# Kernel tuning notes

Hardware: AMD Instinct MI355X
Metric: run time of the kernel (lower is better)

## Reference

```python
import jax, jax.numpy as jnp
import numpy as np

DIM = 4096
N_HEADS = 32
HEAD_DIM = 128
N_KV_HEADS = 8
KV_REPEATS = N_HEADS // N_KV_HEADS
SLIDING_WINDOW = 4096
SEQLEN = 2048
SCALE = HEAD_DIM ** -0.5
NEG = -1e9


def calculate_rope(x, cos, sin):
    # x: [S, H, D]; cos/sin: [S, D//2] applied to interleaved channel pairs
    x1, x2 = x[..., ::2], x[..., 1::2]
    c, s = cos[:, None, :], sin[:, None, :]
    r1 = x1 * c - x2 * s
    r2 = x1 * s + x2 * c
    return jnp.stack([r1, r2], axis=-1).reshape(x.shape)


def setup_inputs() -> dict:
    key = jax.random.key(0)
    ks = jax.random.split(key, 8)
    x = jax.random.normal(ks[0], (SEQLEN, DIM), dtype=jnp.float32)
    # rotary tables
    inv_freq = 1.0 / (10000.0 ** (np.arange(0, HEAD_DIM, 2, dtype=np.float32) / HEAD_DIM))
    t = np.arange(SEQLEN, dtype=np.float32)
    freqs = np.outer(t, inv_freq)  # [S, D/2]
    cos_freq = jnp.asarray(np.cos(freqs), dtype=jnp.float32)
    sin_freq = jnp.asarray(np.sin(freqs), dtype=jnp.float32)
    positions = jnp.arange(SEQLEN, dtype=jnp.int32)
    # causal sliding-window additive mask
    i = np.arange(SEQLEN)[:, None]
    j = np.arange(SEQLEN)[None, :]
    allow = (j <= i) & (j > i - SLIDING_WINDOW)
    mask = jnp.asarray(np.where(allow, 0.0, NEG), dtype=jnp.float32)
    cache_k = jnp.zeros((SLIDING_WINDOW, N_KV_HEADS, HEAD_DIM), dtype=jnp.float32)
    cache_v = jnp.zeros((SLIDING_WINDOW, N_KV_HEADS, HEAD_DIM), dtype=jnp.float32)
    # eqx.nn.Linear weights have shape (out_features, in_features)
    sd = DIM ** -0.5
    wq = jax.random.normal(ks[1], (N_HEADS * HEAD_DIM, DIM), dtype=jnp.float32) * sd
    wk = jax.random.normal(ks[2], (N_KV_HEADS * HEAD_DIM, DIM), dtype=jnp.float32) * sd
    wv = jax.random.normal(ks[3], (N_KV_HEADS * HEAD_DIM, DIM), dtype=jnp.float32) * sd
    wo = jax.random.normal(ks[4], (DIM, N_HEADS * HEAD_DIM), dtype=jnp.float32) * (N_HEADS * HEAD_DIM) ** -0.5
    return {"x": x, "cos_freq": cos_freq, "sin_freq": sin_freq, "positions": positions,
            "mask": mask, "cache_k": cache_k, "cache_v": cache_v,
            "wq": wq, "wk": wk, "wv": wv, "wo": wo}


def reference(x, cos_freq, sin_freq, positions, mask, cache_k, cache_v, wq, wk, wv, wo):
    seqlen = x.shape[0]
    xq = (x @ wq.T).reshape(seqlen, N_HEADS, HEAD_DIM)
    xk = (x @ wk.T).reshape(seqlen, N_KV_HEADS, HEAD_DIM)
    xv = (x @ wv.T).reshape(seqlen, N_KV_HEADS, HEAD_DIM)
    xq = calculate_rope(xq, cos_freq, sin_freq)
    xk = calculate_rope(xk, cos_freq, sin_freq)
    # prefill branch (positions.shape[0] > 1): scatter into sliding-window cache
    cache_k = cache_k.at[positions, :, :].set(xk[positions, :, :], mode='drop')
    cache_v = cache_v.at[positions, :, :].set(xv[positions, :, :], mode='drop')
    # GQA repeat kv heads
    k = jnp.repeat(xk, KV_REPEATS, axis=1)  # [S, H, D]
    v = jnp.repeat(xv, KV_REPEATS, axis=1)
    # scores: [H, Sq, Sk]
    scores = jnp.einsum('qhd,khd->hqk', xq, k) * SCALE
    scores = scores + mask[None, ...]
    probs = jax.nn.softmax(scores.astype(jnp.float32), axis=-1).astype(xq.dtype)
    out = jnp.einsum('hqk,khd->qhd', probs, v).reshape(seqlen, N_HEADS * HEAD_DIM)
    output = out @ wo.T
    return output, cache_k, cache_v
```

## Files before the change

kernel.cpp:

```cpp
#include <hip/hip_runtime.h>

typedef unsigned short ushort_t;
typedef unsigned int uint_t;
typedef __attribute__((ext_vector_type(8))) short bf16x8;
typedef __attribute__((ext_vector_type(4))) float floatx4;

#define SEQ 2048
#define DIM 4096
#define NH 32
#define NKV 8
#define HD 128
#define KVDIM 1024
#define QKVN 6144

__device__ __forceinline__ ushort_t f2b(float f) {
  union { float f; uint_t u; } x; x.f = f;
  uint_t u = x.u;
  u += 0x7fffu + ((u >> 16) & 1u);
  return (ushort_t)(u >> 16);
}

#define GLOAD_LDS(g, l) \
  __builtin_amdgcn_global_load_lds((const __attribute__((address_space(1))) void*)(g), \
                                   (__attribute__((address_space(3))) void*)(l), 16, 0, 0)

__global__ __launch_bounds__(256) void cvt_bf16(const float* __restrict__ src,
                                                ushort_t* __restrict__ dst, int n8) {
  int i = blockIdx.x * 256 + threadIdx.x;
  if (i >= n8) return;
  const float4* s = (const float4*)src;
  float4 a = s[2 * i], b = s[2 * i + 1];
  union { ushort_t u[8]; uint4 v; } o;
  o.u[0] = f2b(a.x); o.u[1] = f2b(a.y); o.u[2] = f2b(a.z); o.u[3] = f2b(a.w);
  o.u[4] = f2b(b.x); o.u[5] = f2b(b.y); o.u[6] = f2b(b.z); o.u[7] = f2b(b.w);
  ((uint4*)dst)[i] = o.v;
}

__global__ __launch_bounds__(256) void gemm128(const ushort_t* __restrict__ A,
                                               const ushort_t* __restrict__ B,
                                               float* __restrict__ C,
                                               int N, int K) {
  __shared__ __attribute__((aligned(16))) ushort_t lds_a[128 * 32];
  __shared__ __attribute__((aligned(16))) ushort_t lds_b[128 * 32];
  int tid = threadIdx.x;
  int lane = tid & 63;
  int w = tid >> 6;
  int m0 = blockIdx.y * 128, n0 = blockIdx.x * 128;
  int wm = (w >> 1) * 64, wn = (w & 1) * 64;
  int row = lane & 15, quad = lane >> 4;

  int sr = tid >> 2;
  int sc = (tid & 3) * 8;
  const ushort_t* Ag = A + (size_t)(m0 + sr) * K + sc;
  const ushort_t* Bg = B + (size_t)(n0 + sr) * K + sc;
  ushort_t* la0 = &lds_a[(tid & ~63) * 8];
  ushort_t* lb0 = &lds_b[(tid & ~63) * 8];

  floatx4 acc[4][4] = {};
  for (int k0 = 0; k0 < K; k0 += 32) {
    GLOAD_LDS(Ag + k0, la0);
    GLOAD_LDS(Ag + (size_t)64 * K + k0, la0 + 2048);
    GLOAD_LDS(Bg + k0, lb0);
    GLOAD_LDS(Bg + (size_t)64 * K + k0, lb0 + 2048);
    __syncthreads();
    bf16x8 af[4], bfr[4];
#pragma unroll
    for (int i = 0; i < 4; ++i) af[i] = *(const bf16x8*)&lds_a[(wm + i * 16 + row) * 32 + quad * 8];
#pragma unroll
    for (int j = 0; j < 4; ++j) bfr[j] = *(const bf16x8*)&lds_b[(wn + j * 16 + row) * 32 + quad * 8];
#pragma unroll
    for (int i = 0; i < 4; ++i)
#pragma unroll
      for (int j = 0; j < 4; ++j)
        acc[i][j] = __builtin_amdgcn_mfma_f32_16x16x32_bf16(af[i], bfr[j], acc[i][j], 0, 0, 0);
    __syncthreads();
  }
#pragma unroll
  for (int i = 0; i < 4; ++i)
#pragma unroll
    for (int j = 0; j < 4; ++j) {
      float* Cp = C + (size_t)(m0 + wm + i * 16 + quad * 4) * N + n0 + wn + j * 16 + row;
#pragma unroll
      for (int r = 0; r < 4; ++r) Cp[(size_t)r * N] = acc[i][j][r];
    }
}

__global__ __launch_bounds__(256) void rope_q(const float* __restrict__ qkv,
                                              const float* __restrict__ cosf,
                                              const float* __restrict__ sinf,
                                              ushort_t* __restrict__ qb) {
  int idx = blockIdx.x * 256 + threadIdx.x;
  int pos = idx >> 11;
  int p = idx & 2047;
  int h = p >> 6, i = p & 63;
  size_t sb = (size_t)pos * QKVN + h * HD + 2 * i;
  float x1 = qkv[sb], x2 = qkv[sb + 1];
  float c = cosf[pos * 64 + i], s = sinf[pos * 64 + i];
  float r1 = x1 * c - x2 * s;
  float r2 = x1 * s + x2 * c;
  size_t db = (size_t)pos * DIM + h * HD + 2 * i;
  ((uint_t*)qb)[db >> 1] = (uint_t)f2b(r1) | ((uint_t)f2b(r2) << 16);
}

__global__ __launch_bounds__(256) void rope_k(const float* __restrict__ qkv,
                                              const float* __restrict__ cosf,
                                              const float* __restrict__ sinf,
                                              ushort_t* __restrict__ kb,
                                              float* __restrict__ cache_k) {
  int idx = blockIdx.x * 256 + threadIdx.x;
  int pos = idx >> 9;
  int p = idx & 511;
  int kvh = p >> 6, i = p & 63;
  size_t sb = (size_t)pos * QKVN + DIM + kvh * HD + 2 * i;
  float x1 = qkv[sb], x2 = qkv[sb + 1];
  float c = cosf[pos * 64 + i], s = sinf[pos * 64 + i];
  float r1 = x1 * c - x2 * s;
  float r2 = x1 * s + x2 * c;
  size_t db = (size_t)pos * KVDIM + kvh * HD + 2 * i;
  ((uint_t*)kb)[db >> 1] = (uint_t)f2b(r1) | ((uint_t)f2b(r2) << 16);
  float2 cv; cv.x = r1; cv.y = r2;
  ((float2*)cache_k)[db >> 1] = cv;
}

__global__ __launch_bounds__(256) void vt_cache(const float* __restrict__ qkv,
                                                ushort_t* __restrict__ vtb,
                                                float* __restrict__ cache_v) {
  __shared__ float tile[64][65];
  int pos0 = blockIdx.x * 64, c0 = blockIdx.y * 64;
  int t = threadIdx.x;
  int pr = t >> 4, cq = (t & 15) * 4;
#pragma unroll
  for (int rr = 0; rr < 4; ++rr) {
    int prow = pr + rr * 16;
    float4 v = *(const float4*)(qkv + (size_t)(pos0 + prow) * QKVN + DIM + KVDIM + c0 + cq);
    *(float4*)(cache_v + (size_t)(pos0 + prow) * KVDIM + c0 + cq) = v;
    tile[prow][cq] = v.x; tile[prow][cq + 1] = v.y;
    tile[prow][cq + 2] = v.z; tile[prow][cq + 3] = v.w;
  }
  __syncthreads();
  int dc = t >> 2, pg = (t & 3) * 16;
  int kvh = c0 >> 7, dl = (c0 & 127) + dc;
  union { ushort_t u[16]; uint4 q[2]; } o;
#pragma unroll
  for (int e = 0; e < 16; ++e) o.u[e] = f2b(tile[pg + e][dc]);
  uint4* dst = (uint4*)(vtb + (size_t)kvh * (HD * SEQ) + (size_t)dl * SEQ + pos0 + pg);
  dst[0] = o.q[0]; dst[1] = o.q[1];
}

__global__ __launch_bounds__(256) void zero_tail(float* __restrict__ out) {
  int i = blockIdx.x * 256 + threadIdx.x;
  float4 z = {0.f, 0.f, 0.f, 0.f};
  ((float4*)(out + 10485760))[i] = z;
  ((float4*)(out + 14680064))[i] = z;
}

__global__ __launch_bounds__(256) void attn(const ushort_t* __restrict__ Q,
                                            const ushort_t* __restrict__ Kb,
                                            const ushort_t* __restrict__ Vt,
                                            ushort_t* __restrict__ O) {
  int qb = 31 - blockIdx.x;
  int h = blockIdx.y;
  int kvh = h >> 2;
  int tid = threadIdx.x;
  int w = tid >> 6, lane = tid & 63;
  int row = lane & 15, quad = lane >> 4;

  __shared__ __attribute__((aligned(16))) ushort_t lds_k[64][136];
  __shared__ __attribute__((aligned(16))) ushort_t lds_vt[128][72];
  __shared__ __attribute__((aligned(16))) float p_lds[4][16][68];

  int q0 = qb * 64 + w * 16;
  bf16x8 qf[4];
  const ushort_t* qp = Q + (size_t)(q0 + row) * DIM + h * HD + quad * 8;
#pragma unroll
  for (int ks = 0; ks < 4; ++ks) qf[ks] = *(const bf16x8*)(qp + ks * 32);

  floatx4 o_acc[8] = {};
  float l_r[4] = {0.f, 0.f, 0.f, 0.f};
  const float ssc = 0.08838834764831845f;

  int kr = tid >> 2, kc = (tid & 3) * 32;
  int vd = tid >> 1, vj = (tid & 1) * 32;
  const ushort_t* kg = Kb + (size_t)kr * KVDIM + kvh * HD + kc;
  const ushort_t* vg = Vt + (size_t)kvh * (HD * SEQ) + (size_t)vd * SEQ + vj;

  for (int kt = 0; kt <= qb; ++kt) {
    int kv0 = kt * 64;
#pragma unroll
    for (int e = 0; e < 4; ++e)
      *(bf16x8*)&lds_k[kr][kc + e * 8] = *(const bf16x8*)(kg + (size_t)kv0 * KVDIM + e * 8);
#pragma unroll
    for (int e = 0; e < 4; ++e)
      *(bf16x8*)&lds_vt[vd][vj + e * 8] = *(const bf16x8*)(vg + kv0 + e * 8);
    __syncthreads();

    floatx4 s[4] = {};
#pragma unroll
    for (int j2 = 0; j2 < 4; ++j2)
#pragma unroll
      for (int ks = 0; ks < 4; ++ks) {
        bf16x8 kfrag = *(const bf16x8*)&lds_k[j2 * 16 + row][ks * 32 + quad * 8];
        s[j2] = __builtin_amdgcn_mfma_f32_16x16x32_bf16(qf[ks], kfrag, s[j2], 0, 0, 0);
      }

    bool diag = (kt == qb);
    float pv[4][4];
#pragma unroll
    for (int j2 = 0; j2 < 4; ++j2)
#pragma unroll
      for (int r = 0; r < 4; ++r) {
        float v = s[j2][r] * ssc;
        if (diag) {
          int j_g = kv0 + j2 * 16 + row;
          int i_g = q0 + quad * 4 + r;
          v += (j_g <= i_g) ? 0.f : -1e9f;
        }
        float p = __expf(v);
        pv[j2][r] = p;
        l_r[r] += p;
      }
#pragma unroll
    for (int j2 = 0; j2 < 4; ++j2)
#pragma unroll
      for (int r = 0; r < 4; ++r) p_lds[w][quad * 4 + r][j2 * 16 + row] = pv[j2][r];
    bf16x8 pf[2];
#pragma unroll
    for (int kb = 0; kb < 2; ++kb) {
      union { bf16x8 v; ushort_t u[8]; } pu;
#pragma unroll
      for (int jj = 0; jj < 8; ++jj) pu.u[jj] = f2b(p_lds[w][row][kb * 32 + quad * 8 + jj]);
      pf[kb] = pu.v;
    }
#pragma unroll
    for (int db = 0; db < 8; ++db)
#pragma unroll
      for (int kb = 0; kb < 2; ++kb) {
        bf16x8 vfrag = *(const bf16x8*)&lds_vt[db * 16 + row][kb * 32 + quad * 8];
        o_acc[db] = __builtin_amdgcn_mfma_f32_16x16x32_bf16(pf[kb], vfrag, o_acc[db], 0, 0, 0);
      }
    __syncthreads();
  }

#pragma unroll
  for (int off = 1; off < 16; off <<= 1)
#pragma unroll
    for (int r = 0; r < 4; ++r) l_r[r] += __shfl_xor(l_r[r], off, 64);
  float inv[4];
#pragma unroll
  for (int r = 0; r < 4; ++r) inv[r] = 1.0f / l_r[r];
#pragma unroll
  for (int db = 0; db < 8; ++db)
#pragma unroll
    for (int r = 0; r < 4; ++r)
      O[(size_t)(q0 + quad * 4 + r) * DIM + h * HD + db * 16 + row] = f2b(o_acc[db][r] * inv[r]);
}

extern "C" void kernel_launch(void* const* d_in, const int* in_sizes, int n_in,
                              void* d_out, int out_size, void* d_ws, size_t ws_size,
                              hipStream_t stream) {
  const float* x    = (const float*)d_in[0];
  const float* cosf = (const float*)d_in[1];
  const float* sinf = (const float*)d_in[2];
  const float* wq = (const float*)d_in[7];
  const float* wk = (const float*)d_in[8];
  const float* wv = (const float*)d_in[9];
  const float* wo = (const float*)d_in[10];
  float* out = (float*)d_out;
  float* cache_k_out = out + 8388608;
  float* cache_v_out = out + 12582912;

  char* ws = (char*)d_ws;
  ushort_t* xb     = (ushort_t*)(ws + 0);
  ushort_t* wqkvb  = (ushort_t*)(ws + 16777216);
  ushort_t* wob    = (ushort_t*)(ws + 67108864);
  float*    qkv32  = (float*)(ws + 100663296);
  ushort_t* qbuf   = (ushort_t*)(ws + 150994944);
  ushort_t* kbuf   = (ushort_t*)(ws + 167772160);
  ushort_t* vtb    = (ushort_t*)(ws + 171966464);
  ushort_t* attnb  = (ushort_t*)(ws + 176160768);

  cvt_bf16<<<4096, 256, 0, stream>>>(x, xb, 1048576);
  cvt_bf16<<<8192, 256, 0, stream>>>(wq, wqkvb, 2097152);
  cvt_bf16<<<2048, 256, 0, stream>>>(wk, wqkvb + 16777216, 524288);
  cvt_bf16<<<2048, 256, 0, stream>>>(wv, wqkvb + 20971520, 524288);
  cvt_bf16<<<8192, 256, 0, stream>>>(wo, wob, 2097152);
  gemm128<<<dim3(48, 16), 256, 0, stream>>>(xb, wqkvb, qkv32, QKVN, DIM);
  rope_q<<<16384, 256, 0, stream>>>(qkv32, cosf, sinf, qbuf);
  rope_k<<<4096, 256, 0, stream>>>(qkv32, cosf, sinf, kbuf, cache_k_out);
  vt_cache<<<dim3(32, 16), 256, 0, stream>>>(qkv32, vtb, cache_v_out);
  zero_tail<<<2048, 256, 0, stream>>>(out);
  attn<<<dim3(32, 32), 256, 0, stream>>>(qbuf, kbuf, vtb, attnb);
  gemm128<<<dim3(32, 16), 256, 0, stream>>>(attnb, wob, out, DIM, DIM);
}
```

Before: 684.8 us.

## Pair causal query tiles per block and fold softmax scale into Q

The attention kernel now processes two query tiles per block (i and 31-i), so every block does equal causal work and the grid halves. The softmax scale times log2(e) is folded into Q during rope so the inner loop uses exp2f without a per-score multiply. P values are read back from LDS with vector loads. Halving the block count reduces parallelism and latency hiding, and each block runs two sequential phases.

```diff
diff --git a/kernel.cpp b/kernel.cpp
--- a/kernel.cpp
+++ b/kernel.cpp
@@ -89,6 +89,7 @@
                                               const float* __restrict__ cosf,
                                               const float* __restrict__ sinf,
                                               ushort_t* __restrict__ qb) {
+  const float QS = 1.4426950408889634f * 0.08838834764831845f;
   int idx = blockIdx.x * 256 + threadIdx.x;
   int pos = idx >> 11;
   int p = idx & 2047;
@@ -96,8 +97,8 @@
   size_t sb = (size_t)pos * QKVN + h * HD + 2 * i;
   float x1 = qkv[sb], x2 = qkv[sb + 1];
   float c = cosf[pos * 64 + i], s = sinf[pos * 64 + i];
-  float r1 = x1 * c - x2 * s;
-  float r2 = x1 * s + x2 * c;
+  float r1 = (x1 * c - x2 * s) * QS;
+  float r2 = (x1 * s + x2 * c) * QS;
   size_t db = (size_t)pos * DIM + h * HD + 2 * i;
   ((uint_t*)qb)[db >> 1] = (uint_t)f2b(r1) | ((uint_t)f2b(r2) << 16);
 }
@@ -158,7 +159,6 @@
                                             const ushort_t* __restrict__ Kb,
                                             const ushort_t* __restrict__ Vt,
                                             ushort_t* __restrict__ O) {
-  int qb = 31 - blockIdx.x;
   int h = blockIdx.y;
   int kvh = h >> 2;
   int tid = threadIdx.x;
@@ -169,90 +169,96 @@
   __shared__ __attribute__((aligned(16))) ushort_t lds_vt[128][72];
   __shared__ __attribute__((aligned(16))) float p_lds[4][16][68];
 
-  int q0 = qb * 64 + w * 16;
-  bf16x8 qf[4];
-  const ushort_t* qp = Q + (size_t)(q0 + row) * DIM + h * HD + quad * 8;
-#pragma unroll
-  for (int ks = 0; ks < 4; ++ks) qf[ks] = *(const bf16x8*)(qp + ks * 32);
-
-  floatx4 o_acc[8] = {};
-  float l_r[4] = {0.f, 0.f, 0.f, 0.f};
-  const float ssc = 0.08838834764831845f;
-
   int kr = tid >> 2, kc = (tid & 3) * 32;
   int vd = tid >> 1, vj = (tid & 1) * 32;
   const ushort_t* kg = Kb + (size_t)kr * KVDIM + kvh * HD + kc;
   const ushort_t* vg = Vt + (size_t)kvh * (HD * SEQ) + (size_t)vd * SEQ + vj;
 
-  for (int kt = 0; kt <= qb; ++kt) {
-    int kv0 = kt * 64;
-#pragma unroll
-    for (int e = 0; e < 4; ++e)
-      *(bf16x8*)&lds_k[kr][kc + e * 8] = *(const bf16x8*)(kg + (size_t)kv0 * KVDIM + e * 8);
-#pragma unroll
-    for (int e = 0; e < 4; ++e)
-      *(bf16x8*)&lds_vt[vd][vj + e * 8] = *(const bf16x8*)(vg + kv0 + e * 8);
-    __syncthreads();
-
-    floatx4 s[4] = {};
-#pragma unroll
-    for (int j2 = 0; j2 < 4; ++j2)
-#pragma unroll
-      for (int ks = 0; ks < 4; ++ks) {
-        bf16x8 kfrag = *(const bf16x8*)&lds_k[j2 * 16 + row][ks * 32 + quad * 8];
-        s[j2] = __builtin_amdgcn_mfma_f32_16x16x32_bf16(qf[ks], kfrag, s[j2], 0, 0, 0);
+#pragma unroll 1
+  for (int ph = 0; ph < 2; ++ph) {
+    int qb = ph ? (31 - blockIdx.x) : blockIdx.x;
+    int q0 = qb * 64 + w * 16;
+
+    bf16x8 qf[4];
+    const ushort_t* qp = Q + (size_t)(q0 + row) * DIM + h * HD + quad * 8;
+#pragma unroll
+    for (int ks = 0; ks < 4; ++ks) qf[ks] = *(const bf16x8*)(qp + ks * 32);
+
+    floatx4 o_acc[8] = {};
+    float l_r[4] = {0.f, 0.f, 0.f, 0.f};
+
+    for (int kt = 0; kt <= qb; ++kt) {
+      int kv0 = kt * 64;
+#pragma unroll
+      for (int e = 0; e < 4; ++e)
+        *(bf16x8*)&lds_k[kr][kc + e * 8] = *(const bf16x8*)(kg + (size_t)kv0 * KVDIM + e * 8);
+#pragma unroll
+      for (int e = 0; e < 4; ++e)
+        *(bf16x8*)&lds_vt[vd][vj + e * 8] = *(const bf16x8*)(vg + kv0 + e * 8);
+      __syncthreads();
+
+      floatx4 s[4] = {};
+#pragma unroll
+      for (int j2 = 0; j2 < 4; ++j2)
+#pragma unroll
+        for (int ks = 0; ks < 4; ++ks) {
+          bf16x8 kfrag = *(const bf16x8*)&lds_k[j2 * 16 + row][ks * 32 + quad * 8];
+          s[j2] = __builtin_amdgcn_mfma_f32_16x16x32_bf16(qf[ks], kfrag, s[j2], 0, 0, 0);
+        }
+
+      bool diag = (kt == qb);
+      float pv[4][4];
+#pragma unroll
+      for (int j2 = 0; j2 < 4; ++j2)
+#pragma unroll
+        for (int r = 0; r < 4; ++r) {
+          float v = s[j2][r];
+          if (diag) {
+            int j_g = kv0 + j2 * 16 + row;
+            int i_g = q0 + quad * 4 + r;
+            v += (j_g <= i_g) ? 0.f : -1e9f;
+          }
+          float p = exp2f(v);
+          pv[j2][r] = p;
+          l_r[r] += p;
+        }
+#pragma unroll
+      for (int j2 = 0; j2 < 4; ++j2)
+#pragma unroll
+        for (int r = 0; r < 4; ++r) p_lds[w][quad * 4 + r][j2 * 16 + row] = pv[j2][r];
+      bf16x8 pf[2];
+#pragma unroll
+      for (int kb2 = 0; kb2 < 2; ++kb2) {
+        float4 pa = *(const float4*)&p_lds[w][row][kb2 * 32 + quad * 8];
+        float4 pb = *(const float4*)&p_lds[w][row][kb2 * 32 + quad * 8 + 4];
+        union { bf16x8 v; ushort_t u[8]; } pu;
+        pu.u[0] = f2b(pa.x); pu.u[1] = f2b(pa.y); pu.u[2] = f2b(pa.z); pu.u[3] = f2b(pa.w);
+        pu.u[4] = f2b(pb.x); pu.u[5] = f2b(pb.y); pu.u[6] = f2b(pb.z); pu.u[7] = f2b(pb.w);
+        pf[kb2] = pu.v;
       }
-
-    bool diag = (kt == qb);
-    float pv[4][4];
-#pragma unroll
-    for (int j2 = 0; j2 < 4; ++j2)
-#pragma unroll
-      for (int r = 0; r < 4; ++r) {
-        float v = s[j2][r] * ssc;
-        if (diag) {
-          int j_g = kv0 + j2 * 16 + row;
-          int i_g = q0 + quad * 4 + r;
-          v += (j_g <= i_g) ? 0.f : -1e9f;
+#pragma unroll
+      for (int db = 0; db < 8; ++db)
+#pragma unroll
+        for (int kb2 = 0; kb2 < 2; ++kb2) {
+          bf16x8 vfrag = *(const bf16x8*)&lds_vt[db * 16 + row][kb2 * 32 + quad * 8];
+          o_acc[db] = __builtin_amdgcn_mfma_f32_16x16x32_bf16(pf[kb2], vfrag, o_acc[db], 0, 0, 0);
         }
-        float p = __expf(v);
-        pv[j2][r] = p;
-        l_r[r] += p;
-      }
-#pragma unroll
-    for (int j2 = 0; j2 < 4; ++j2)
-#pragma unroll
-      for (int r = 0; r < 4; ++r) p_lds[w][quad * 4 + r][j2 * 16 + row] = pv[j2][r];
-    bf16x8 pf[2];
-#pragma unroll
-    for (int kb = 0; kb < 2; ++kb) {
-      union { bf16x8 v; ushort_t u[8]; } pu;
-#pragma unroll
-      for (int jj = 0; jj < 8; ++jj) pu.u[jj] = f2b(p_lds[w][row][kb * 32 + quad * 8 + jj]);
-      pf[kb] = pu.v;
+      __syncthreads();
     }
+
+#pragma unroll
+    for (int off = 1; off < 16; off <<= 1)
+#pragma unroll
+      for (int r = 0; r < 4; ++r) l_r[r] += __shfl_xor(l_r[r], off, 64);
+    float inv[4];
+#pragma unroll
+    for (int r = 0; r < 4; ++r) inv[r] = 1.0f / l_r[r];
 #pragma unroll
     for (int db = 0; db < 8; ++db)
 #pragma unroll
-      for (int kb = 0; kb < 2; ++kb) {
-        bf16x8 vfrag = *(const bf16x8*)&lds_vt[db * 16 + row][kb * 32 + quad * 8];
-        o_acc[db] = __builtin_amdgcn_mfma_f32_16x16x32_bf16(pf[kb], vfrag, o_acc[db], 0, 0, 0);
-      }
-    __syncthreads();
+      for (int r = 0; r < 4; ++r)
+        O[(size_t)(q0 + quad * 4 + r) * DIM + h * HD + db * 16 + row] = f2b(o_acc[db][r] * inv[r]);
   }
-
-#pragma unroll
-  for (int off = 1; off < 16; off <<= 1)
-#pragma unroll
-    for (int r = 0; r < 4; ++r) l_r[r] += __shfl_xor(l_r[r], off, 64);
-  float inv[4];
-#pragma unroll
-  for (int r = 0; r < 4; ++r) inv[r] = 1.0f / l_r[r];
-#pragma unroll
-  for (int db = 0; db < 8; ++db)
-#pragma unroll
-    for (int r = 0; r < 4; ++r)
-      O[(size_t)(q0 + quad * 4 + r) * DIM + h * HD + db * 16 + row] = f2b(o_acc[db][r] * inv[r]);
 }
 
 extern "C" void kernel_launch(void* const* d_in, const int* in_sizes, int n_in,
@@ -289,6 +295,6 @@
   rope_k<<<4096, 256, 0, stream>>>(qkv32, cosf, sinf, kbuf, cache_k_out);
   vt_cache<<<dim3(32, 16), 256, 0, stream>>>(qkv32, vtb, cache_v_out);
   zero_tail<<<2048, 256, 0, stream>>>(out);
-  attn<<<dim3(32, 32), 256, 0, stream>>>(qbuf, kbuf, vtb, attnb);
+  attn<<<dim3(16, 32), 256, 0, stream>>>(qbuf, kbuf, vtb, attnb);
   gemm128<<<dim3(32, 16), 256, 0, stream>>>(attnb, wob, out, DIM, DIM);
 }
```

Result: faster. 622.0 us (-9.2%).
